# Performance work log

Hardware: AMD Instinct MI355X
Metric: run time of the kernel (lower is better)

The kernel has to match this reference:

```python
import jax, jax.numpy as jnp
import numpy as np

SUB_NO = 20
T_NO = 201
E_NO = 2000
I_NO = 500
T_DATA = 20000

def _make_cden():
    C = np.zeros((SUB_NO, SUB_NO), dtype=np.float32)
    for i in range(SUB_NO):
        for c in (2 * i + 1, 2 * i + 2):
            if c < SUB_NO:
                C[i, c] = 1.0
    return C

C_DEN = _make_cden()
CHILDREN = [np.where(C_DEN[s] == 1)[0] for s in range(SUB_NO)]  # static tree structure


def setup_inputs() -> dict:
    key = jax.random.key(0)
    ks = jax.random.split(key, 12)
    eps = 1e-6
    inp = {}
    inp['S_e'] = jax.random.uniform(ks[0], (T_DATA, E_NO), dtype=jnp.float32)
    inp['S_i'] = jax.random.uniform(ks[1], (T_DATA, I_NO), dtype=jnp.float32)
    # uniform noise for REBAR reparam; clipped away from {0,1} so log(-log(u)) is finite
    inp['u'] = jnp.clip(jax.random.uniform(ks[2], (SUB_NO, E_NO + I_NO), dtype=jnp.float32), eps, 1.0 - eps)
    inp['v'] = jnp.clip(jax.random.uniform(ks[3], (SUB_NO, E_NO + I_NO), dtype=jnp.float32), eps, 1.0 - eps)
    inp['W_syn'] = jax.random.normal(ks[4], (SUB_NO, 2), dtype=jnp.float32) * 0.1
    inp['Tau_syn'] = jnp.ones((SUB_NO, 2), dtype=jnp.float32)
    inp['Delta_syn'] = jax.random.uniform(ks[5], (SUB_NO, 2), dtype=jnp.float32)
    inp['W_sub'] = jax.random.uniform(ks[6], (SUB_NO,), dtype=jnp.float32)
    inp['V_o'] = jax.random.normal(ks[7], (1,), dtype=jnp.float32)
    inp['Theta'] = jnp.zeros((SUB_NO,), dtype=jnp.float32)
    inp['C_syn_log'] = jnp.ones((SUB_NO, E_NO + I_NO), dtype=jnp.float32)
    return inp


def _H(x):
    # one-hot of per-column argmax (first max, as torch.argmax)
    idx = jnp.argmax(x, axis=0)
    return jax.nn.one_hot(idx, x.shape[0], axis=0, dtype=x.dtype)


def _reparam_pz(u, theta):
    return jnp.log(theta) - jnp.log(-jnp.log(u))


def _reparam_pz_b(v, b, theta):
    # b is one-hot per column; v_k = v at the b==1 row of each column
    v_k = jnp.sum(v * b, axis=0, keepdims=True)  # [1, cols]
    z_same = -jnp.log(-jnp.log(v))
    z_diff = -jnp.log(-jnp.log(v) / theta - jnp.log(v_k))
    return b * z_same + (1.0 - b) * z_diff


def _evaluate_f(C_syn, S_e, S_i, W_syn, Tau_syn, Delta_syn, W_sub, V_o):
    T_data = S_e.shape[0]
    C_syn_e = C_syn[:, :E_NO]          # [sub, E]
    C_syn_i = C_syn[:, -I_NO:]         # [sub, I]
    # double-exponential (alpha) synaptic kernels, vectorized over subunits & e/i
    t_raw = jnp.arange(T_NO, dtype=S_e.dtype)                               # [T_no]
    t = jnp.maximum(t_raw[None, None, :] - jnp.exp(Delta_syn)[:, :, None], 0.0)  # [sub,2,T_no]
    t_tau = t / jnp.exp(Tau_syn)[:, :, None]
    kern = t_tau * jnp.exp(-t_tau) * W_syn[:, :, None]                      # [sub,2,T_no]
    # project spikes onto subunits
    in_e = S_e @ C_syn_e.T   # [T, sub]
    in_i = S_i @ C_syn_i.T   # [T, sub]
    # causal depthwise conv: syn[t,s] = sum_tau kern[s,:,tau] * in[t-tau,s]
    inp = jnp.stack([in_e.T, in_i.T], axis=1).reshape(1, SUB_NO * 2, T_data)   # NCH
    k = jnp.flip(kern, axis=-1).reshape(SUB_NO * 2, 1, T_NO)                   # OIH
    filt = jax.lax.conv_general_dilated(
        inp, k, window_strides=(1,), padding=[(T_NO - 1, 0)],
        feature_group_count=SUB_NO * 2,
        dimension_numbers=('NCH', 'OIH', 'NCH'))
    syn_in = filt.reshape(SUB_NO, 2, T_data).sum(axis=1).T   # [T, sub]
    # tree-recurrent tanh aggregation (children have higher index than parents)
    sub_out = [None] * SUB_NO
    for s in range(SUB_NO):
        idx = SUB_NO - 1 - s
        ch = CHILDREN[idx]
        if ch.size == 0:
            sub_out[idx] = jnp.tanh(syn_in[:, idx])
        else:
            leaf = sum(sub_out[c] * W_sub[c] for c in ch)
            sub_out[idx] = jnp.tanh(syn_in[:, idx] + leaf)
    return sub_out[0] * W_sub[0] + V_o[0]


def reference(S_e, S_i, u, v, W_syn, Tau_syn, Delta_syn, W_sub, V_o, Theta, C_syn_log):
    theta = jax.nn.softmax(C_syn_log, axis=0)
    rebar_z = _reparam_pz(u, theta)
    hard_z = _H(rebar_z)
    rebar_zb = _reparam_pz_b(v, hard_z, theta)
    soft_z = jax.nn.sigmoid(rebar_z / 0.5) + 1e-9
    soft_zb = jax.nn.sigmoid(rebar_zb / 0.5) + 1e-9
    V_hard_z = _evaluate_f(hard_z, S_e, S_i, W_syn, Tau_syn, Delta_syn, W_sub, V_o)
    V_soft_z = _evaluate_f(soft_z, S_e, S_i, W_syn, Tau_syn, Delta_syn, W_sub, V_o)
    V_soft_zb = _evaluate_f(soft_zb, S_e, S_i, W_syn, Tau_syn, Delta_syn, W_sub, V_o)
    return (V_hard_z, V_soft_z, V_soft_zb, theta, hard_z, soft_z, soft_zb)
```

## Files before the change

kernel.cpp:

```cpp
#include <hip/hip_runtime.h>
#include <math.h>

#define SUBS 20
#define TAPS 201
#define ENO 2000
#define INO 500
#define TDATA 20000

typedef __bf16 bf16x8 __attribute__((ext_vector_type(8)));
typedef float f32x4 __attribute__((ext_vector_type(4)));

#define WGE_STRIDE 2048
#define WGI_STRIDE 512

#define WGE_OFF  0ull
#define WGI_OFF  262144ull
#define KERN_OFF 327680ull
#define INE_OFF  360448ull
#define INI_OFF  (INE_OFF + 4800000ull)
#define P1_OFF   (INI_OFF + 4800000ull)
#define P2_OFF   (P1_OFF  + 4800000ull)
#define P3_OFF   (P2_OFF  + 4800000ull)
#define SYN_OFF  (P3_OFF  + 4800000ull)

__device__ __forceinline__ unsigned short f2bf(float f) {
  union { float f; unsigned int u; } c; c.f = f;
  unsigned int u = c.u;
  return (unsigned short)((u + 0x7FFFu + ((u >> 16) & 1u)) >> 16);
}

__device__ __forceinline__ float fast_tanh(float x) {
  const float ax = fabsf(x);
  const float e  = __expf(2.f * ax);
  const float t  = 1.f - 2.f / (e + 1.f);
  return copysignf(t, x);
}

__global__ __launch_bounds__(256) void prep_kernel(
    const float* __restrict__ u, const float* __restrict__ v,
    const float* __restrict__ C_log, const float* __restrict__ W_syn,
    const float* __restrict__ Tau_syn, const float* __restrict__ Delta_syn,
    float* __restrict__ out,
    unsigned short* __restrict__ wge, unsigned short* __restrict__ wgi,
    float* __restrict__ kern)
{
  if (blockIdx.x < 10) {
    const int n = blockIdx.x * 256 + threadIdx.x;
    if (n >= 2500) return;
    float x[SUBS], theta[SUBS], rebar[SUBS];
    float mx = -1e30f;
#pragma unroll
    for (int s = 0; s < SUBS; ++s) { x[s] = C_log[s*2500 + n]; mx = fmaxf(mx, x[s]); }
    float sum = 0.f;
#pragma unroll
    for (int s = 0; s < SUBS; ++s) { theta[s] = __expf(x[s] - mx); sum += theta[s]; }
    const float inv = 1.f / sum;
    int idx = 0; float best = -1e30f;
#pragma unroll
    for (int s = 0; s < SUBS; ++s) {
      theta[s] *= inv;
      out[60000 + s*2500 + n] = theta[s];
      const float uu = u[s*2500 + n];
      const float r = __logf(theta[s]) - __logf(-__logf(uu));
      rebar[s] = r;
      if (r > best) { best = r; idx = s; }
    }
    const float lvk = __logf(v[idx*2500 + n]);
#pragma unroll
    for (int s = 0; s < SUBS; ++s) {
      const float hz = (s == idx) ? 1.f : 0.f;
      const float sz = 1.f / (1.f + __expf(-2.f * rebar[s])) + 1e-9f;
      const float vv = v[s*2500 + n];
      const float zb = (s == idx) ? (-__logf(-__logf(vv)))
                                  : (-__logf(-__logf(vv) / theta[s] - lvk));
      const float szb = 1.f / (1.f + __expf(-2.f * zb)) + 1e-9f;
      out[110000 + s*2500 + n] = hz;
      out[160000 + s*2500 + n] = sz;
      out[210000 + s*2500 + n] = szb;
      if (n < ENO) {
        wge[(s     )*WGE_STRIDE + n] = f2bf(hz);
        wge[(20 + s)*WGE_STRIDE + n] = f2bf(sz);
        wge[(40 + s)*WGE_STRIDE + n] = f2bf(szb);
      } else {
        const int k = n - ENO;
        wgi[(s     )*WGI_STRIDE + k] = f2bf(hz);
        wgi[(20 + s)*WGI_STRIDE + k] = f2bf(sz);
        wgi[(40 + s)*WGI_STRIDE + k] = f2bf(szb);
      }
    }
  } else {
    const int tid = threadIdx.x;
    for (int i = tid; i < 40*TAPS; i += 256) {
      const int ch = i / TAPS, m = i - ch*TAPS;
      const float dl  = __expf(Delta_syn[ch]);
      const float tau = __expf(Tau_syn[ch]);
      const float t  = fmaxf((float)m - dl, 0.f);
      const float tt = t / tau;
      kern[i] = tt * __expf(-tt) * W_syn[ch];
    }
    for (int i = tid; i < 4*2048; i += 256) wge[(60 + (i >> 11))*WGE_STRIDE + (i & 2047)] = 0;
    for (int i = tid; i < 60*48;  i += 256) wge[(i / 48)*WGE_STRIDE + 2000 + (i % 48)] = 0;
    for (int i = tid; i < 4*512;  i += 256) wgi[(60 + (i >> 9))*WGI_STRIDE + (i & 511)] = 0;
    for (int i = tid; i < 60*12;  i += 256) wgi[(i / 12)*WGI_STRIDE + 500 + (i % 12)] = 0;
  }
}

__device__ __forceinline__ void gl16(float4& d, const void* p) {
  asm volatile("global_load_dwordx4 %0, %1, off"
               : "=&v"(d) : "v"(p) : "memory");
}

#define MFMA_B16 __builtin_amdgcn_mfma_f32_16x16x32_bf16
#define BC8(x) __builtin_bit_cast(bf16x8, x)

__global__ __launch_bounds__(256) void gemm_kernel(
    const float* __restrict__ S_e, const float* __restrict__ S_i,
    const unsigned short* __restrict__ wge, const unsigned short* __restrict__ wgi,
    float* __restrict__ in_e, float* __restrict__ in_i,
    float* __restrict__ P1, float* __restrict__ P2, float* __restrict__ P3)
{
  const int tid  = threadIdx.x;
  const int wave = tid >> 6;
  const int lane = tid & 63;
  const int m16  = lane & 15;
  const int quad = lane >> 4;
  const int kq   = quad * 8;
  const int t0   = blockIdx.x * 64;
  const int cy   = blockIdx.y;
  const bool isE = (cy < 4);

  const float* S = isE ? S_e : S_i;
  const unsigned short* Wg = isE ? wge : wgi;
  float* outp = (cy == 0) ? in_e : (cy == 1) ? P1 : (cy == 2) ? P2
              : (cy == 3) ? P3   : in_i;
  const int K       = isE ? ENO : INO;
  const int Wstride = isE ? WGE_STRIDE : WGI_STRIDE;
  const int k_base  = isE ? cy * 512 : 0;

  const int tA = t0 + wave*16 + m16;
  const float* Arow = S + (size_t)((tA < TDATA) ? tA : TDATA - 1) * K;
  const unsigned short* B0 = Wg + (size_t)(m16     ) * Wstride;
  const unsigned short* B1 = Wg + (size_t)(m16 + 16) * Wstride;
  const unsigned short* B2 = Wg + (size_t)(m16 + 32) * Wstride;
  const unsigned short* B3 = Wg + (size_t)(m16 + 48) * Wstride;

  f32x4 acc0 = {0.f,0.f,0.f,0.f};
  f32x4 acc1 = acc0, acc2 = acc0, acc3 = acc0;

  float4 a00,a01,a02,a03, b00,b01,b02,b03,b04,b05,b06,b07;
  float4 a10,a11,a12,a13, b10,b11,b12,b13,b14,b15,b16,b17;

#define ISSUE(ST, A0,A1,A2,A3, Q0,Q1,Q2,Q3,Q4,Q5,Q6,Q7) do {            \
    const int k0_ = k_base + (ST)*64 + kq;                              \
    const int k1_ = k0_ + 32;                                           \
    gl16(Q0, B0 + k0_); gl16(Q1, B1 + k0_);                             \
    gl16(Q2, B2 + k0_); gl16(Q3, B3 + k0_);                             \
    gl16(Q4, B0 + k1_); gl16(Q5, B1 + k1_);                             \
    gl16(Q6, B2 + k1_); gl16(Q7, B3 + k1_);                             \
    const int c0_ = (k0_     <= K - 4) ? k0_     : K - 4;               \
    const int c1_ = (k0_ + 4 <= K - 4) ? k0_ + 4 : K - 4;               \
    const int c2_ = (k1_     <= K - 4) ? k1_     : K - 4;               \
    const int c3_ = (k1_ + 4 <= K - 4) ? k1_ + 4 : K - 4;               \
    gl16(A0, Arow + c0_); gl16(A1, Arow + c1_);                         \
    gl16(A2, Arow + c2_); gl16(A3, Arow + c3_);                         \
  } while (0)

#define WAITN(N) do {                                                   \
    asm volatile("s_waitcnt vmcnt(" #N ")" ::: "memory");               \
    __builtin_amdgcn_sched_barrier(0);                                  \
  } while (0)

#define COMPUTE(A0,A1,A2,A3, Q0,Q1,Q2,Q3,Q4,Q5,Q6,Q7) do {              \
    bf16x8 x0, x1;                                                      \
    x0[0]=(__bf16)A0.x; x0[1]=(__bf16)A0.y;                             \
    x0[2]=(__bf16)A0.z; x0[3]=(__bf16)A0.w;                             \
    x0[4]=(__bf16)A1.x; x0[5]=(__bf16)A1.y;                             \
    x0[6]=(__bf16)A1.z; x0[7]=(__bf16)A1.w;                             \
    x1[0]=(__bf16)A2.x; x1[1]=(__bf16)A2.y;                             \
    x1[2]=(__bf16)A2.z; x1[3]=(__bf16)A2.w;                             \
    x1[4]=(__bf16)A3.x; x1[5]=(__bf16)A3.y;                             \
    x1[6]=(__bf16)A3.z; x1[7]=(__bf16)A3.w;                             \
    acc0 = MFMA_B16(x0, BC8(Q0), acc0, 0, 0, 0);                        \
    acc1 = MFMA_B16(x0, BC8(Q1), acc1, 0, 0, 0);                        \
    acc2 = MFMA_B16(x0, BC8(Q2), acc2, 0, 0, 0);                        \
    acc3 = MFMA_B16(x0, BC8(Q3), acc3, 0, 0, 0);                        \
    acc0 = MFMA_B16(x1, BC8(Q4), acc0, 0, 0, 0);                        \
    acc1 = MFMA_B16(x1, BC8(Q5), acc1, 0, 0, 0);                        \
    acc2 = MFMA_B16(x1, BC8(Q6), acc2, 0, 0, 0);                        \
    acc3 = MFMA_B16(x1, BC8(Q7), acc3, 0, 0, 0);                        \
  } while (0)

  ISSUE(0, a00,a01,a02,a03, b00,b01,b02,b03,b04,b05,b06,b07);
  ISSUE(1, a10,a11,a12,a13, b10,b11,b12,b13,b14,b15,b16,b17);
  WAITN(12);
  COMPUTE(a00,a01,a02,a03, b00,b01,b02,b03,b04,b05,b06,b07);
  ISSUE(2, a00,a01,a02,a03, b00,b01,b02,b03,b04,b05,b06,b07);
  WAITN(12);
  COMPUTE(a10,a11,a12,a13, b10,b11,b12,b13,b14,b15,b16,b17);
  ISSUE(3, a10,a11,a12,a13, b10,b11,b12,b13,b14,b15,b16,b17);
  WAITN(12);
  COMPUTE(a00,a01,a02,a03, b00,b01,b02,b03,b04,b05,b06,b07);
  ISSUE(4, a00,a01,a02,a03, b00,b01,b02,b03,b04,b05,b06,b07);
  WAITN(12);
  COMPUTE(a10,a11,a12,a13, b10,b11,b12,b13,b14,b15,b16,b17);
  ISSUE(5, a10,a11,a12,a13, b10,b11,b12,b13,b14,b15,b16,b17);
  WAITN(12);
  COMPUTE(a00,a01,a02,a03, b00,b01,b02,b03,b04,b05,b06,b07);
  ISSUE(6, a00,a01,a02,a03, b00,b01,b02,b03,b04,b05,b06,b07);
  WAITN(12);
  COMPUTE(a10,a11,a12,a13, b10,b11,b12,b13,b14,b15,b16,b17);
  ISSUE(7, a10,a11,a12,a13, b10,b11,b12,b13,b14,b15,b16,b17);
  WAITN(12);
  COMPUTE(a00,a01,a02,a03, b00,b01,b02,b03,b04,b05,b06,b07);
  WAITN(0);
  COMPUTE(a10,a11,a12,a13, b10,b11,b12,b13,b14,b15,b16,b17);

#undef ISSUE
#undef WAITN
#undef COMPUTE

  const int t = t0 + wave*16 + quad*4;
  if (t < TDATA) {
    float* o = outp + t;
    *(float4*)(o + (size_t)(     m16)*TDATA) = *(float4*)&acc0;
    *(float4*)(o + (size_t)(16 + m16)*TDATA) = *(float4*)&acc1;
    *(float4*)(o + (size_t)(32 + m16)*TDATA) = *(float4*)&acc2;
    if (m16 < 12)
      *(float4*)(o + (size_t)(48 + m16)*TDATA) = *(float4*)&acc3;
  }
}

__device__ __forceinline__ int swz(int i) { return i + (i >> 5); }

__global__ __launch_bounds__(256) void conv_kernel(
    const float* __restrict__ in_e, const float* __restrict__ P1,
    const float* __restrict__ P2,  const float* __restrict__ P3,
    const float* __restrict__ in_i,
    const float* __restrict__ kern, float* __restrict__ syn)
{
  __shared__ float Ee[2320];
  __shared__ float Ei[2320];
  const int ch = blockIdx.y;
  const int t0 = blockIdx.x * 2048;
  const int s  = ch % SUBS;
  const size_t off = (size_t)ch * TDATA;
  for (int i = threadIdx.x; i < 2248; i += 256) {
    const int g = t0 - 200 + i;
    float e = 0.f, ii = 0.f;
    if (g >= 0 && g < TDATA) {
      e = in_e[off + g] + P1[off + g] + P2[off + g] + P3[off + g];
      ii = in_i[off + g];
    }
    Ee[swz(i)] = e;
    Ei[swz(i)] = ii;
  }
  __syncthreads();
  const float* ke = kern + (size_t)(s*2    ) * TAPS;
  const float* ki = kern + (size_t)(s*2 + 1) * TAPS;
  const int tb = threadIdx.x * 8;
  float acc[8] = {0.f,0.f,0.f,0.f,0.f,0.f,0.f,0.f};
  float we[8], wi[8];
#pragma unroll
  for (int j = 0; j < 8; ++j) {
    we[j] = Ee[swz(tb + 200 + j)];
    wi[j] = Ei[swz(tb + 200 + j)];
  }
#pragma unroll 8
  for (int m = 0; m < TAPS; ++m) {
    const float k0 = ke[m];
    const float k1 = ki[m];
#pragma unroll
    for (int j = 0; j < 8; ++j)
      acc[j] = fmaf(we[j], k0, fmaf(wi[j], k1, acc[j]));
    if (m < TAPS - 1) {
#pragma unroll
      for (int j = 7; j > 0; --j) { we[j] = we[j-1]; wi[j] = wi[j-1]; }
      we[0] = Ee[swz(tb + 199 - m)];
      wi[0] = Ei[swz(tb + 199 - m)];
    }
  }
  const int t = t0 + tb;
  if (t < TDATA) {
    float* o = syn + off + t;
    *(float4*)(o    ) = make_float4(acc[0], acc[1], acc[2], acc[3]);
    *(float4*)(o + 4) = make_float4(acc[4], acc[5], acc[6], acc[7]);
  }
}

__global__ __launch_bounds__(256) void tree_kernel(
    const float* __restrict__ syn, const float* __restrict__ W_sub,
    const float* __restrict__ V_o, float* __restrict__ out)
{
  const int t = blockIdx.x * 256 + threadIdx.x;
  const int var = blockIdx.y;
  if (t >= TDATA) return;
  const float* sp = syn + (size_t)var * SUBS * TDATA + t;
  float so[SUBS];
#pragma unroll
  for (int s = SUBS - 1; s >= 0; --s) {
    float val = sp[(size_t)s * TDATA];
    const int c1 = 2*s + 1, c2 = 2*s + 2;
    if (c1 < SUBS) val += so[c1] * W_sub[c1];
    if (c2 < SUBS) val += so[c2] * W_sub[c2];
    so[s] = fast_tanh(val);
  }
  out[(size_t)var * TDATA + t] = so[0] * W_sub[0] + V_o[0];
}

extern "C" void kernel_launch(void* const* d_in, const int* in_sizes, int n_in,
                              void* d_out, int out_size, void* d_ws, size_t ws_size,
                              hipStream_t stream) {
  const float* S_e     = (const float*)d_in[0];
  const float* S_i     = (const float*)d_in[1];
  const float* u       = (const float*)d_in[2];
  const float* v       = (const float*)d_in[3];
  const float* W_syn   = (const float*)d_in[4];
  const float* Tau_syn = (const float*)d_in[5];
  const float* Delta   = (const float*)d_in[6];
  const float* W_sub   = (const float*)d_in[7];
  const float* V_o     = (const float*)d_in[8];
  const float* C_log   = (const float*)d_in[10];
  float* out = (float*)d_out;
  char* ws = (char*)d_ws;
  unsigned short* wge = (unsigned short*)(ws + WGE_OFF);
  unsigned short* wgi = (unsigned short*)(ws + WGI_OFF);
  float* kern = (float*)(ws + KERN_OFF);
  float* in_e = (float*)(ws + INE_OFF);
  float* in_i = (float*)(ws + INI_OFF);
  float* P1   = (float*)(ws + P1_OFF);
  float* P2   = (float*)(ws + P2_OFF);
  float* P3   = (float*)(ws + P3_OFF);
  float* syn  = (float*)(ws + SYN_OFF);

  prep_kernel<<<dim3(11), dim3(256), 0, stream>>>(u, v, C_log, W_syn, Tau_syn,
                                                  Delta, out, wge, wgi, kern);
  gemm_kernel<<<dim3(313, 5), dim3(256), 0, stream>>>(
      S_e, S_i, wge, wgi, in_e, in_i, P1, P2, P3);
  conv_kernel<<<dim3(10, 60), dim3(256), 0, stream>>>(in_e, P1, P2, P3, in_i,
                                                      kern, syn);
  tree_kernel<<<dim3(79, 3), dim3(256), 0, stream>>>(syn, W_sub, V_o, out);
}
```

Baseline: 334.3 us.

## Stage A tile through LDS with coalesced row loads and bf16 conversion

The GEMM kernel now loads each wave's 16 rows of S with coalesced 16-byte loads (lanes span contiguous K), converts them to bf16, and stores them in a padded per-wave LDS buffer. The MFMA loop then reads A fragments from LDS, while B stays in registers fetched from global memory. This replaces strided per-row A loads that touched scattered 32-byte pieces and left poor coalescing, at the cost of LDS usage (about 66KB per block), which may lower occupancy, and a full prologue before compute begins. The WAITN counts change because each stage now only waits on the B loads.

```diff
diff --git a/kernel.cpp b/kernel.cpp
--- a/kernel.cpp
+++ b/kernel.cpp
@@ -27,6 +27,11 @@
   union { float f; unsigned int u; } c; c.f = f;
   unsigned int u = c.u;
   return (unsigned short)((u + 0x7FFFu + ((u >> 16) & 1u)) >> 16);
+}
+
+__device__ __forceinline__ ushort4 cvt4(float4 f) {
+  ushort4 q; q.x = f2bf(f.x); q.y = f2bf(f.y);
+  q.z = f2bf(f.z); q.w = f2bf(f.w); return q;
 }
 
 __device__ __forceinline__ float fast_tanh(float x) {
@@ -119,12 +124,13 @@
     float* __restrict__ in_e, float* __restrict__ in_i,
     float* __restrict__ P1, float* __restrict__ P2, float* __restrict__ P3)
 {
+  __shared__ unsigned short Alds[4][16][520];
   const int tid  = threadIdx.x;
   const int wave = tid >> 6;
   const int lane = tid & 63;
   const int m16  = lane & 15;
   const int quad = lane >> 4;
-  const int kq   = quad * 8;
+  const int l4   = lane * 4;
   const int t0   = blockIdx.x * 64;
   const int cy   = blockIdx.y;
   const bool isE = (cy < 4);
@@ -137,49 +143,82 @@
   const int Wstride = isE ? WGE_STRIDE : WGI_STRIDE;
   const int k_base  = isE ? cy * 512 : 0;
 
-  const int tA = t0 + wave*16 + m16;
-  const float* Arow = S + (size_t)((tA < TDATA) ? tA : TDATA - 1) * K;
+  const int kq0 = k_base + l4;
+  const int kq1 = k_base + 256 + l4;
+  const int c0  = (kq0 <= K - 4) ? kq0 : K - 4;
+  const int c1  = (kq1 <= K - 4) ? kq1 : K - 4;
+
+  const float* Rp[16];
+#pragma unroll
+  for (int r = 0; r < 16; ++r) {
+    const int tr = t0 + wave*16 + r;
+    Rp[r] = S + (size_t)((tr < TDATA) ? tr : TDATA - 1) * K;
+  }
+
   const unsigned short* B0 = Wg + (size_t)(m16     ) * Wstride;
   const unsigned short* B1 = Wg + (size_t)(m16 + 16) * Wstride;
   const unsigned short* B2 = Wg + (size_t)(m16 + 32) * Wstride;
   const unsigned short* B3 = Wg + (size_t)(m16 + 48) * Wstride;
 
+#define WAITN(N) do {                                                   \
+    asm volatile("s_waitcnt vmcnt(" #N ")" ::: "memory");               \
+    __builtin_amdgcn_sched_barrier(0);                                  \
+  } while (0)
+
+#define SLOAD(R, d0,d1,d2,d3,d4,d5,d6,d7) do {                          \
+    gl16(d0, Rp[(R)    ] + c0); gl16(d1, Rp[(R)    ] + c1);             \
+    gl16(d2, Rp[(R) + 1] + c0); gl16(d3, Rp[(R) + 1] + c1);             \
+    gl16(d4, Rp[(R) + 2] + c0); gl16(d5, Rp[(R) + 2] + c1);             \
+    gl16(d6, Rp[(R) + 3] + c0); gl16(d7, Rp[(R) + 3] + c1);             \
+  } while (0)
+
+#define SSTORE(R, d0,d1,d2,d3,d4,d5,d6,d7) do {                         \
+    *(ushort4*)&Alds[wave][(R)    ][      l4] = cvt4(d0);               \
+    *(ushort4*)&Alds[wave][(R)    ][256 + l4] = cvt4(d1);               \
+    *(ushort4*)&Alds[wave][(R) + 1][      l4] = cvt4(d2);               \
+    *(ushort4*)&Alds[wave][(R) + 1][256 + l4] = cvt4(d3);               \
+    *(ushort4*)&Alds[wave][(R) + 2][      l4] = cvt4(d4);               \
+    *(ushort4*)&Alds[wave][(R) + 2][256 + l4] = cvt4(d5);               \
+    *(ushort4*)&Alds[wave][(R) + 3][      l4] = cvt4(d6);               \
+    *(ushort4*)&Alds[wave][(R) + 3][256 + l4] = cvt4(d7);               \
+  } while (0)
+
+  {
+    float4 gA0,gA1,gA2,gA3,gA4,gA5,gA6,gA7;
+    float4 gB0,gB1,gB2,gB3,gB4,gB5,gB6,gB7;
+    float4 gC0,gC1,gC2,gC3,gC4,gC5,gC6,gC7;
+    float4 gD0,gD1,gD2,gD3,gD4,gD5,gD6,gD7;
+    SLOAD(0,  gA0,gA1,gA2,gA3,gA4,gA5,gA6,gA7);
+    SLOAD(4,  gB0,gB1,gB2,gB3,gB4,gB5,gB6,gB7);
+    WAITN(8);
+    SSTORE(0, gA0,gA1,gA2,gA3,gA4,gA5,gA6,gA7);
+    SLOAD(8,  gC0,gC1,gC2,gC3,gC4,gC5,gC6,gC7);
+    WAITN(8);
+    SSTORE(4, gB0,gB1,gB2,gB3,gB4,gB5,gB6,gB7);
+    SLOAD(12, gD0,gD1,gD2,gD3,gD4,gD5,gD6,gD7);
+    WAITN(8);
+    SSTORE(8, gC0,gC1,gC2,gC3,gC4,gC5,gC6,gC7);
+    WAITN(0);
+    SSTORE(12,gD0,gD1,gD2,gD3,gD4,gD5,gD6,gD7);
+  }
+#undef SLOAD
+#undef SSTORE
+
   f32x4 acc0 = {0.f,0.f,0.f,0.f};
   f32x4 acc1 = acc0, acc2 = acc0, acc3 = acc0;
 
-  float4 a00,a01,a02,a03, b00,b01,b02,b03,b04,b05,b06,b07;
-  float4 a10,a11,a12,a13, b10,b11,b12,b13,b14,b15,b16,b17;
-
-#define ISSUE(ST, A0,A1,A2,A3, Q0,Q1,Q2,Q3,Q4,Q5,Q6,Q7) do {            \
-    const int k0_ = k_base + (ST)*64 + kq;                              \
+#define ISSUE_B(ST, Q0,Q1,Q2,Q3,Q4,Q5,Q6,Q7) do {                       \
+    const int k0_ = k_base + (ST)*64 + quad*8;                          \
     const int k1_ = k0_ + 32;                                           \
     gl16(Q0, B0 + k0_); gl16(Q1, B1 + k0_);                             \
     gl16(Q2, B2 + k0_); gl16(Q3, B3 + k0_);                             \
     gl16(Q4, B0 + k1_); gl16(Q5, B1 + k1_);                             \
     gl16(Q6, B2 + k1_); gl16(Q7, B3 + k1_);                             \
-    const int c0_ = (k0_     <= K - 4) ? k0_     : K - 4;               \
-    const int c1_ = (k0_ + 4 <= K - 4) ? k0_ + 4 : K - 4;               \
-    const int c2_ = (k1_     <= K - 4) ? k1_     : K - 4;               \
-    const int c3_ = (k1_ + 4 <= K - 4) ? k1_ + 4 : K - 4;               \
-    gl16(A0, Arow + c0_); gl16(A1, Arow + c1_);                         \
-    gl16(A2, Arow + c2_); gl16(A3, Arow + c3_);                         \
-  } while (0)
-
-#define WAITN(N) do {                                                   \
-    asm volatile("s_waitcnt vmcnt(" #N ")" ::: "memory");               \
-    __builtin_amdgcn_sched_barrier(0);                                  \
-  } while (0)
-
-#define COMPUTE(A0,A1,A2,A3, Q0,Q1,Q2,Q3,Q4,Q5,Q6,Q7) do {              \
-    bf16x8 x0, x1;                                                      \
-    x0[0]=(__bf16)A0.x; x0[1]=(__bf16)A0.y;                             \
-    x0[2]=(__bf16)A0.z; x0[3]=(__bf16)A0.w;                             \
-    x0[4]=(__bf16)A1.x; x0[5]=(__bf16)A1.y;                             \
-    x0[6]=(__bf16)A1.z; x0[7]=(__bf16)A1.w;                             \
-    x1[0]=(__bf16)A2.x; x1[1]=(__bf16)A2.y;                             \
-    x1[2]=(__bf16)A2.z; x1[3]=(__bf16)A2.w;                             \
-    x1[4]=(__bf16)A3.x; x1[5]=(__bf16)A3.y;                             \
-    x1[6]=(__bf16)A3.z; x1[7]=(__bf16)A3.w;                             \
+  } while (0)
+
+#define COMPUTE(ST, Q0,Q1,Q2,Q3,Q4,Q5,Q6,Q7) do {                       \
+    const bf16x8 x0 = *(const bf16x8*)&Alds[wave][m16][(ST)*64      + quad*8]; \
+    const bf16x8 x1 = *(const bf16x8*)&Alds[wave][m16][(ST)*64 + 32 + quad*8]; \
     acc0 = MFMA_B16(x0, BC8(Q0), acc0, 0, 0, 0);                        \
     acc1 = MFMA_B16(x0, BC8(Q1), acc1, 0, 0, 0);                        \
     acc2 = MFMA_B16(x0, BC8(Q2), acc2, 0, 0, 0);                        \
@@ -190,34 +229,37 @@
     acc3 = MFMA_B16(x1, BC8(Q7), acc3, 0, 0, 0);                        \
   } while (0)
 
-  ISSUE(0, a00,a01,a02,a03, b00,b01,b02,b03,b04,b05,b06,b07);
-  ISSUE(1, a10,a11,a12,a13, b10,b11,b12,b13,b14,b15,b16,b17);
-  WAITN(12);
-  COMPUTE(a00,a01,a02,a03, b00,b01,b02,b03,b04,b05,b06,b07);
-  ISSUE(2, a00,a01,a02,a03, b00,b01,b02,b03,b04,b05,b06,b07);
-  WAITN(12);
-  COMPUTE(a10,a11,a12,a13, b10,b11,b12,b13,b14,b15,b16,b17);
-  ISSUE(3, a10,a11,a12,a13, b10,b11,b12,b13,b14,b15,b16,b17);
-  WAITN(12);
-  COMPUTE(a00,a01,a02,a03, b00,b01,b02,b03,b04,b05,b06,b07);
-  ISSUE(4, a00,a01,a02,a03, b00,b01,b02,b03,b04,b05,b06,b07);
-  WAITN(12);
-  COMPUTE(a10,a11,a12,a13, b10,b11,b12,b13,b14,b15,b16,b17);
-  ISSUE(5, a10,a11,a12,a13, b10,b11,b12,b13,b14,b15,b16,b17);
-  WAITN(12);
-  COMPUTE(a00,a01,a02,a03, b00,b01,b02,b03,b04,b05,b06,b07);
-  ISSUE(6, a00,a01,a02,a03, b00,b01,b02,b03,b04,b05,b06,b07);
-  WAITN(12);
-  COMPUTE(a10,a11,a12,a13, b10,b11,b12,b13,b14,b15,b16,b17);
-  ISSUE(7, a10,a11,a12,a13, b10,b11,b12,b13,b14,b15,b16,b17);
-  WAITN(12);
-  COMPUTE(a00,a01,a02,a03, b00,b01,b02,b03,b04,b05,b06,b07);
-  WAITN(0);
-  COMPUTE(a10,a11,a12,a13, b10,b11,b12,b13,b14,b15,b16,b17);
-
-#undef ISSUE
+  {
+    float4 s00,s01,s02,s03,s04,s05,s06,s07;
+    float4 s10,s11,s12,s13,s14,s15,s16,s17;
+    ISSUE_B(0, s00,s01,s02,s03,s04,s05,s06,s07);
+    ISSUE_B(1, s10,s11,s12,s13,s14,s15,s16,s17);
+    WAITN(8);
+    COMPUTE(0, s00,s01,s02,s03,s04,s05,s06,s07);
+    ISSUE_B(2, s00,s01,s02,s03,s04,s05,s06,s07);
+    WAITN(8);
+    COMPUTE(1, s10,s11,s12,s13,s14,s15,s16,s17);
+    ISSUE_B(3, s10,s11,s12,s13,s14,s15,s16,s17);
+    WAITN(8);
+    COMPUTE(2, s00,s01,s02,s03,s04,s05,s06,s07);
+    ISSUE_B(4, s00,s01,s02,s03,s04,s05,s06,s07);
+    WAITN(8);
+    COMPUTE(3, s10,s11,s12,s13,s14,s15,s16,s17);
+    ISSUE_B(5, s10,s11,s12,s13,s14,s15,s16,s17);
+    WAITN(8);
+    COMPUTE(4, s00,s01,s02,s03,s04,s05,s06,s07);
+    ISSUE_B(6, s00,s01,s02,s03,s04,s05,s06,s07);
+    WAITN(8);
+    COMPUTE(5, s10,s11,s12,s13,s14,s15,s16,s17);
+    ISSUE_B(7, s10,s11,s12,s13,s14,s15,s16,s17);
+    WAITN(8);
+    COMPUTE(6, s00,s01,s02,s03,s04,s05,s06,s07);
+    WAITN(0);
+    COMPUTE(7, s10,s11,s12,s13,s14,s15,s16,s17);
+  }
+#undef ISSUE_B
+#undef COMPUTE
 #undef WAITN
-#undef COMPUTE
 
   const int t = t0 + wave*16 + quad*4;
   if (t < TDATA) {
```

Result: slower. 347.0 us (+3.8%).
